# Kernel tuning notes

Measured on AMD Instinct MI355X. Metric: run time of the kernel, lower is better.

## Reference

```python
import jax, jax.numpy as jnp
import numpy as np

B, C, H, W, KS = 8, 3, 512, 512, 3
K = KS * KS  # kernel_elements = 9


def setup_inputs() -> dict:
    key = jax.random.key(0)
    ks = jax.random.split(key, 5)
    return {
        "x": jax.random.normal(ks[0], (B, C, H, W), jnp.float32),
        "w1": jax.random.normal(ks[1], (K - 1, C, KS, KS), jnp.float32) * 0.1,  # find_ref conv weight
        "b1": jax.random.normal(ks[2], (K - 1,), jnp.float32) * 0.1,
        "w2": jax.random.normal(ks[3], (C, K), jnp.float32) * 0.1,  # grouped 1x1 conv: C groups, K in-ch each
        "b2": jax.random.normal(ks[4], (C,), jnp.float32) * 0.1,
    }


def _grid_sample_bilinear(img_nhwc, gx, gy):
    # torch.grid_sample, mode='bilinear', padding_mode='zeros', align_corners=False
    # img_nhwc: [B,H,W,C]; gx,gy: [B,h,w,K] normalized coords (x=width, y=height)
    Bs, Hh, Ww, _ = img_nhwc.shape
    ix = ((gx + 1.0) * Ww - 1.0) * 0.5
    iy = ((gy + 1.0) * Hh - 1.0) * 0.5
    ix0 = jnp.floor(ix)
    iy0 = jnp.floor(iy)
    wx1 = ix - ix0
    wy1 = iy - iy0
    wx0 = 1.0 - wx1
    wy0 = 1.0 - wy1
    bidx = jnp.arange(Bs)[:, None, None, None]

    def corner(yc, xc, wgt):
        valid = (xc >= 0) & (xc < Ww) & (yc >= 0) & (yc < Hh)
        xi = jnp.clip(xc, 0, Ww - 1).astype(jnp.int32)
        yi = jnp.clip(yc, 0, Hh - 1).astype(jnp.int32)
        v = img_nhwc[bidx, yi, xi]  # [B,h,w,K,C]
        return v * (wgt * valid)[..., None]

    out = corner(iy0, ix0, wy0 * wx0)
    out = out + corner(iy0, ix0 + 1.0, wy0 * wx1)
    out = out + corner(iy0 + 1.0, ix0, wy1 * wx0)
    out = out + corner(iy0 + 1.0, ix0 + 1.0, wy1 * wx1)
    return out  # [B,h,w,K,C]


def _forward(x, w1, b1, w2, b2):
    Bs, Cc, Hh, Ww = x.shape
    pad = KS // 2
    # find_ref: conv3x3 (pad=1) + sigmoid -> offsets in [0,1]
    off = jax.lax.conv_general_dilated(
        x, w1, (1, 1), ((pad, pad), (pad, pad)),
        dimension_numbers=("NCHW", "OIHW", "NCHW"))
    off = jax.nn.sigmoid(off + b1[None, :, None, None])  # [B,K-1,H,W]
    off = jnp.transpose(off, (0, 2, 3, 1)).reshape(Bs, Hh, Ww, (K - 1) // 2, 2)
    ctr = float(KS // 2)
    sym = 2.0 * ctr - off  # find_symmetric_points
    center = jnp.zeros((Bs, Hh, Ww, 1, 2), off.dtype)
    off_all = jnp.concatenate([off, center, sym], axis=-2)  # [B,H,W,K,2]
    # base grid: stack(h_grid, w_grid) with linspace(0,1)
    base = jnp.stack(
        jnp.meshgrid(jnp.linspace(0.0, 1.0, Hh), jnp.linspace(0.0, 1.0, Ww), indexing="ij"),
        axis=-1)  # [H,W,2]
    coords = base[None, :, :, None, :] + off_all  # [B,H,W,K,2]
    # grid_sample interprets last dim as (x=width, y=height)
    gx = coords[..., 0]
    gy = coords[..., 1]
    img = jnp.transpose(x, (0, 2, 3, 1))  # [B,H,W,C]
    sampled = _grid_sample_bilinear(img, gx, gy)  # [B,H,W,K,C]
    # concatenation order in torch: elem-major channels -> [B, K*C, H, W]
    deformed = jnp.transpose(sampled, (0, 3, 4, 1, 2)).reshape(Bs, K * Cc, Hh, Ww)
    # grouped 1x1 conv: groups=C, group g consumes channels [g*K:(g+1)*K]
    grp = deformed.reshape(Bs, Cc, K, Hh, Ww)
    out = jnp.einsum("bgkhw,gk->bghw", grp, w2) + b2[None, :, None, None]
    return jax.nn.relu(out)


def reference(x, w1, b1, w2, b2):
    return _forward(x, w1, b1, w2, b2)
```

## Files before the change

### kernel.cpp

```cpp
#include <hip/hip_runtime.h>

#define BATCH 8
#define HDIM  512
#define WDIM  512
#define PLANE (HDIM * WDIM)

typedef _Float16 half4v __attribute__((ext_vector_type(4)));
typedef _Float16 half8v __attribute__((ext_vector_type(8)));

struct __align__(8) HPair { half4v lo, hi; };

__global__ __launch_bounds__(256) void repack_h4(
    const float* __restrict__ x,
    half8v* __restrict__ xp)
{
    int gid = blockIdx.x * 256 + threadIdx.x;
    int b = gid >> 17;
    int u = gid & ((PLANE / 2) - 1);
    const float* xb = x + (size_t)b * 3 * PLANE;
    int pix = u * 2;
    float2 a0 = *(const float2*)(xb + pix);
    float2 a1 = *(const float2*)(xb + PLANE + pix);
    float2 a2 = *(const float2*)(xb + 2 * PLANE + pix);
    half8v o;
    o[0] = (_Float16)a0.x; o[1] = (_Float16)a1.x; o[2] = (_Float16)a2.x; o[3] = (_Float16)0.f;
    o[4] = (_Float16)a0.y; o[5] = (_Float16)a1.y; o[6] = (_Float16)a2.y; o[7] = (_Float16)0.f;
    xp[(size_t)gid] = o;
}

__device__ __forceinline__ void gather5(
    const half4v* __restrict__ hb, const float* __restrict__ w2,
    const float s[8], float bx, float by, float og[3])
{
    int   adr[5][2];
    float wY[5][2], wX0[5], wX1[5];
#pragma unroll
    for (int q = 0; q < 5; q++) {
        float c0 = (q < 4) ? s[2 * q]     : 0.0f;
        float c1 = (q < 4) ? s[2 * q + 1] : 0.0f;
        float ixf = fmaf(bx + c0, 256.0f, 255.5f);
        float iyf = fmaf(by + c1, 256.0f, 255.5f);
        float ix0f = floorf(ixf);
        float iy0f = floorf(iyf);
        float wx1 = ixf - ix0f, wy1 = iyf - iy0f;
        float wx0 = 1.f - wx1,  wy0 = 1.f - wy1;
        int ix0 = (int)ix0f, iy0 = (int)iy0f;

        float wx0v = (ix0 <= 511) ? wx0 : 0.f;
        float wx1v = (ix0 <= 510) ? wx1 : 0.f;
        float wy0v = (iy0 <= 511) ? wy0 : 0.f;
        float wy1v = (iy0 <= 510) ? wy1 : 0.f;
        int x0c = min(ix0, 511);
        int y0c = min(iy0, 511), y1c = min(iy0 + 1, 511);

        float wxs = wx0v + wx1v;
        wX0[q] = wx0v; wX1[q] = wx1v;
        wY[q][0] = wy0v; wY[q][1] = wy1v;
        adr[q][0] = (wy0v * wxs > 0.f) ? ((y0c << 9) + x0c) : 0;
        adr[q][1] = (wy1v * wxs > 0.f) ? ((y1c << 9) + x0c) : 0;
    }

    HPair pv[5][2];
#pragma unroll
    for (int q = 0; q < 5; q++) {
        pv[q][0] = *(const HPair*)(hb + adr[q][0]);
        pv[q][1] = *(const HPair*)(hb + adr[q][1]);
    }

#pragma unroll
    for (int q = 0; q < 5; q++) {
        float sc[3];
#pragma unroll
        for (int c = 0; c < 3; c++) {
            float r0 = fmaf((float)pv[q][0].hi[c], wX1[q], (float)pv[q][0].lo[c] * wX0[q]);
            float r1 = fmaf((float)pv[q][1].hi[c], wX1[q], (float)pv[q][1].lo[c] * wX0[q]);
            sc[c] = fmaf(r1, wY[q][1], r0 * wY[q][0]);
        }
        int g  = q / 3;
        int k0 = (q % 3) * 3;
        og[g] = fmaf(sc[0], w2[g * 9 + k0 + 0], og[g]);
        og[g] = fmaf(sc[1], w2[g * 9 + k0 + 1], og[g]);
        og[g] = fmaf(sc[2], w2[g * 9 + k0 + 2], og[g]);
    }
}

__global__ __launch_bounds__(256) void seesaw_v4(
    const float* __restrict__ x,
    const half4v* __restrict__ xp,
    const float* __restrict__ w1, const float* __restrict__ b1,
    const float* __restrict__ w2, const float* __restrict__ b2,
    float* __restrict__ out)
{
    int t = threadIdx.x;
    int gid = blockIdx.x * 256 + t;
    int u  = gid & 255;
    int j0 = u << 1;
    int i  = (gid >> 8) & 511;
    int b  = gid >> 17;

    const float*  xb = x  + (size_t)b * 3 * PLANE;
    const half4v* hb = xp + ((size_t)b << 18);

    float accA[8], accB[8];
#pragma unroll
    for (int e = 0; e < 8; e++) { accA[e] = b1[e]; accB[e] = b1[e]; }

#pragma unroll
    for (int di = 0; di < 3; di++) {
        int y = i + di - 1;
        bool yv = (unsigned)y < (unsigned)HDIM;
        int yc = yv ? y : 0;
#pragma unroll
        for (int dx = 0; dx < 4; dx++) {
            int xc = j0 + dx - 1;
            bool xv = (unsigned)xc < (unsigned)WDIM;
            int xcc = xv ? xc : 0;
            int base = (yc << 9) + xcc;
            float v0 = xb[base];
            float v1 = xb[PLANE + base];
            float v2 = xb[2 * PLANE + base];
            if (!(yv && xv)) { v0 = 0.f; v1 = 0.f; v2 = 0.f; }
#pragma unroll
            for (int e = 0; e < 8; e++) {
                if (dx < 3) {
                    accA[e] = fmaf(v0, w1[e * 27 +      di * 3 + dx], accA[e]);
                    accA[e] = fmaf(v1, w1[e * 27 +  9 + di * 3 + dx], accA[e]);
                    accA[e] = fmaf(v2, w1[e * 27 + 18 + di * 3 + dx], accA[e]);
                }
                if (dx >= 1) {
                    accB[e] = fmaf(v0, w1[e * 27 +      di * 3 + dx - 1], accB[e]);
                    accB[e] = fmaf(v1, w1[e * 27 +  9 + di * 3 + dx - 1], accB[e]);
                    accB[e] = fmaf(v2, w1[e * 27 + 18 + di * 3 + dx - 1], accB[e]);
                }
            }
        }
    }

    float sA[8], sB[8];
#pragma unroll
    for (int e = 0; e < 8; e++) {
        sA[e] = __builtin_amdgcn_rcpf(1.0f + __expf(-accA[e]));
        sB[e] = __builtin_amdgcn_rcpf(1.0f + __expf(-accB[e]));
    }

    const float inv511 = 1.0f / 511.0f;
    float bx  = (float)i * inv511;
    float byA = (float)j0 * inv511;
    float byB = (float)(j0 + 1) * inv511;

    float ogA[3] = {0.f, 0.f, 0.f};
    float ogB[3] = {0.f, 0.f, 0.f};
    gather5(hb, w2, sA, bx, byA, ogA);
    gather5(hb, w2, sB, bx, byB, ogB);

    if ((i | u) == 0) {
#pragma unroll
        for (int p = 5; p < 9; p++) {
            float c0 = 2.0f - sA[2 * (p - 5)];
            float c1 = 2.0f - sA[2 * (p - 5) + 1];
            float ixf = fmaf(bx + c0, 256.0f, 255.5f);
            float iyf = fmaf(byA + c1, 256.0f, 255.5f);
            float ix0f = floorf(ixf), iy0f = floorf(iyf);
            float wx1 = ixf - ix0f, wy1 = iyf - iy0f;
            float wx0 = 1.f - wx1,  wy0 = 1.f - wy1;
            int ix0 = (int)ix0f, iy0 = (int)iy0f;
            float s0 = 0.f, s1 = 0.f, s2 = 0.f;
            for (int cy = 0; cy < 2; cy++) {
                int yc2 = iy0 + cy;
                if (yc2 < 0 || yc2 >= HDIM) continue;
                float wy = cy ? wy1 : wy0;
                for (int cx = 0; cx < 2; cx++) {
                    int xcc2 = ix0 + cx;
                    if (xcc2 < 0 || xcc2 >= WDIM) continue;
                    float wgt = wy * (cx ? wx1 : wx0);
                    int base = (yc2 << 9) + xcc2;
                    s0 = fmaf(xb[base],             wgt, s0);
                    s1 = fmaf(xb[PLANE + base],     wgt, s1);
                    s2 = fmaf(xb[2 * PLANE + base], wgt, s2);
                }
            }
            int g  = p / 3;
            int k0 = (p % 3) * 3;
            ogA[g] = fmaf(s0, w2[g * 9 + k0 + 0], ogA[g]);
            ogA[g] = fmaf(s1, w2[g * 9 + k0 + 1], ogA[g]);
            ogA[g] = fmaf(s2, w2[g * 9 + k0 + 2], ogA[g]);
        }
    }

    size_t ob = (size_t)(b * 3) * PLANE + ((size_t)i << 9) + j0;
#pragma unroll
    for (int g = 0; g < 3; g++) {
        float va = ogA[g] + b2[g];
        float vb = ogB[g] + b2[g];
        float2 o2;
        o2.x = va > 0.f ? va : 0.f;
        o2.y = vb > 0.f ? vb : 0.f;
        *(float2*)(out + ob + (size_t)g * PLANE) = o2;
    }
}

__global__ __launch_bounds__(256) void seesaw_fused_v1(
    const float* __restrict__ x, const float* __restrict__ w1,
    const float* __restrict__ b1, const float* __restrict__ w2,
    const float* __restrict__ b2, float* __restrict__ out)
{
    int t = threadIdx.x;
    int gid = blockIdx.x * 256 + t;
    int j = gid & (WDIM - 1);
    int i = (gid >> 9) & (HDIM - 1);
    int b = gid >> 18;
    const float* xb = x + (size_t)b * 3 * PLANE;
    float acc[8];
#pragma unroll
    for (int e = 0; e < 8; e++) acc[e] = b1[e];
#pragma unroll
    for (int di = 0; di < 3; di++) {
        int y = i + di - 1;
        if (y < 0 || y >= HDIM) continue;
#pragma unroll
        for (int dj = 0; dj < 3; dj++) {
            int xc = j + dj - 1;
            if (xc < 0 || xc >= WDIM) continue;
            size_t base = (size_t)y * WDIM + xc;
#pragma unroll
            for (int c = 0; c < 3; c++) {
                float v = xb[(size_t)c * PLANE + base];
#pragma unroll
                for (int e = 0; e < 8; e++)
                    acc[e] = fmaf(v, w1[e * 27 + c * 9 + di * 3 + dj], acc[e]);
            }
        }
    }
    float s[8];
#pragma unroll
    for (int e = 0; e < 8; e++) s[e] = 1.0f / (1.0f + __expf(-acc[e]));
    const float inv511 = 1.0f / 511.0f;
    float bx = (float)i * inv511, by = (float)j * inv511;
    float og0 = 0.f, og1 = 0.f, og2 = 0.f;
#pragma unroll
    for (int p = 0; p < 9; p++) {
        float c0, c1;
        if (p < 4)       { c0 = s[2 * p];              c1 = s[2 * p + 1]; }
        else if (p == 4) { c0 = 0.f;                   c1 = 0.f; }
        else             { c0 = 2.0f - s[2 * (p - 5)]; c1 = 2.0f - s[2 * (p - 5) + 1]; }
        float ixf = (bx + c0) * 256.0f + 255.5f;
        float iyf = (by + c1) * 256.0f + 255.5f;
        float ix0f = floorf(ixf), iy0f = floorf(iyf);
        float wx1 = ixf - ix0f, wy1 = iyf - iy0f;
        float wx0 = 1.f - wx1,  wy0 = 1.f - wy1;
        int ix0 = (int)ix0f, iy0 = (int)iy0f;
        float s0 = 0.f, s1 = 0.f, s2 = 0.f;
#pragma unroll
        for (int cy = 0; cy < 2; cy++) {
            int yc = iy0 + cy;
            if (yc < 0 || yc >= HDIM) continue;
            float wy = cy ? wy1 : wy0;
#pragma unroll
            for (int cx = 0; cx < 2; cx++) {
                int xcc = ix0 + cx;
                if (xcc < 0 || xcc >= WDIM) continue;
                float wgt = wy * (cx ? wx1 : wx0);
                size_t base = (size_t)yc * WDIM + xcc;
                s0 = fmaf(xb[base],             wgt, s0);
                s1 = fmaf(xb[PLANE + base],     wgt, s1);
                s2 = fmaf(xb[2 * PLANE + base], wgt, s2);
            }
        }
        int g  = p / 3;
        int k0 = (p % 3) * 3;
        float* og = (g == 0) ? &og0 : (g == 1) ? &og1 : &og2;
        *og = fmaf(s0, w2[g * 9 + k0 + 0], *og);
        *og = fmaf(s1, w2[g * 9 + k0 + 1], *og);
        *og = fmaf(s2, w2[g * 9 + k0 + 2], *og);
    }
    size_t ob = (size_t)(b * 3) * PLANE + (size_t)i * WDIM + j;
    float v0 = og0 + b2[0], v1 = og1 + b2[1], v2 = og2 + b2[2];
    out[ob]             = v0 > 0.f ? v0 : 0.f;
    out[ob + PLANE]     = v1 > 0.f ? v1 : 0.f;
    out[ob + 2 * PLANE] = v2 > 0.f ? v2 : 0.f;
}

extern "C" void kernel_launch(void* const* d_in, const int* in_sizes, int n_in,
                              void* d_out, int out_size, void* d_ws, size_t ws_size,
                              hipStream_t stream) {
    const float* x  = (const float*)d_in[0];
    const float* w1 = (const float*)d_in[1];
    const float* b1 = (const float*)d_in[2];
    const float* w2 = (const float*)d_in[3];
    const float* b2 = (const float*)d_in[4];
    float* out = (float*)d_out;

    int total = BATCH * HDIM * WDIM;
    size_t need = (size_t)total * 8 + 16;

    if (ws_size >= need) {
        half8v* xp = (half8v*)d_ws;
        repack_h4<<<total / 2 / 256, 256, 0, stream>>>(x, xp);
        seesaw_v4<<<total / 2 / 256, 256, 0, stream>>>(x, (const half4v*)d_ws,
                                                       w1, b1, w2, b2, out);
    } else {
        seesaw_fused_v1<<<total / 256, 256, 0, stream>>>(x, w1, b1, w2, b2, out);
    }
}
```

Baseline: 139.1 us.

## Fold grouped 1x1 weights into fp16 dot2 gathers and widen repack

The 1x1 grouped-conv weights are now applied to the packed fp16 channel pairs with fdot2 before bilinear interpolation. This replaces per-channel interpolation followed by a weighted sum, cutting ALU work per sample. The two gather5 calls are merged into one 10-point loop, so all 20 gather loads are issued before any math, giving more loads in flight at the cost of more registers. The repack kernel now handles 4 pixels per thread with float4 loads. The main risk is extra rounding error from fp16 weights.

```diff
diff --git a/kernel.cpp b/kernel.cpp
--- a/kernel.cpp
+++ b/kernel.cpp
@@ -5,88 +5,43 @@
 #define WDIM  512
 #define PLANE (HDIM * WDIM)
 
+typedef _Float16 half2v __attribute__((ext_vector_type(2)));
 typedef _Float16 half4v __attribute__((ext_vector_type(4)));
 typedef _Float16 half8v __attribute__((ext_vector_type(8)));
 
-struct __align__(8) HPair { half4v lo, hi; };
-
-__global__ __launch_bounds__(256) void repack_h4(
+struct __align__(8) HQuad { half2v p0, p1, p2, p3; };
+
+#if __has_builtin(__builtin_amdgcn_fdot2)
+#define FDOT2(a, b, c) __builtin_amdgcn_fdot2((a), (b), (c), false)
+#else
+#define FDOT2(a, b, c) fmaf((float)(a).x, (float)(b).x, fmaf((float)(a).y, (float)(b).y, (c)))
+#endif
+
+__global__ __launch_bounds__(256) void repack_h4w(
     const float* __restrict__ x,
     half8v* __restrict__ xp)
 {
     int gid = blockIdx.x * 256 + threadIdx.x;
-    int b = gid >> 17;
-    int u = gid & ((PLANE / 2) - 1);
+    int b = gid >> 16;
+    int u = gid & 65535;
     const float* xb = x + (size_t)b * 3 * PLANE;
-    int pix = u * 2;
-    float2 a0 = *(const float2*)(xb + pix);
-    float2 a1 = *(const float2*)(xb + PLANE + pix);
-    float2 a2 = *(const float2*)(xb + 2 * PLANE + pix);
-    half8v o;
-    o[0] = (_Float16)a0.x; o[1] = (_Float16)a1.x; o[2] = (_Float16)a2.x; o[3] = (_Float16)0.f;
-    o[4] = (_Float16)a0.y; o[5] = (_Float16)a1.y; o[6] = (_Float16)a2.y; o[7] = (_Float16)0.f;
-    xp[(size_t)gid] = o;
+    int pix = u << 2;
+    float4 a0 = *(const float4*)(xb + pix);
+    float4 a1 = *(const float4*)(xb + PLANE + pix);
+    float4 a2 = *(const float4*)(xb + 2 * PLANE + pix);
+    half8v o0, o1;
+    o0[0] = (_Float16)a0.x; o0[1] = (_Float16)a1.x; o0[2] = (_Float16)a2.x; o0[3] = (_Float16)0.f;
+    o0[4] = (_Float16)a0.y; o0[5] = (_Float16)a1.y; o0[6] = (_Float16)a2.y; o0[7] = (_Float16)0.f;
+    o1[0] = (_Float16)a0.z; o1[1] = (_Float16)a1.z; o1[2] = (_Float16)a2.z; o1[3] = (_Float16)0.f;
+    o1[4] = (_Float16)a0.w; o1[5] = (_Float16)a1.w; o1[6] = (_Float16)a2.w; o1[7] = (_Float16)0.f;
+    size_t base = (size_t)b * (PLANE / 2) + (size_t)u * 2;
+    xp[base]     = o0;
+    xp[base + 1] = o1;
 }
 
-__device__ __forceinline__ void gather5(
-    const half4v* __restrict__ hb, const float* __restrict__ w2,
-    const float s[8], float bx, float by, float og[3])
-{
-    int   adr[5][2];
-    float wY[5][2], wX0[5], wX1[5];
-#pragma unroll
-    for (int q = 0; q < 5; q++) {
-        float c0 = (q < 4) ? s[2 * q]     : 0.0f;
-        float c1 = (q < 4) ? s[2 * q + 1] : 0.0f;
-        float ixf = fmaf(bx + c0, 256.0f, 255.5f);
-        float iyf = fmaf(by + c1, 256.0f, 255.5f);
-        float ix0f = floorf(ixf);
-        float iy0f = floorf(iyf);
-        float wx1 = ixf - ix0f, wy1 = iyf - iy0f;
-        float wx0 = 1.f - wx1,  wy0 = 1.f - wy1;
-        int ix0 = (int)ix0f, iy0 = (int)iy0f;
-
-        float wx0v = (ix0 <= 511) ? wx0 : 0.f;
-        float wx1v = (ix0 <= 510) ? wx1 : 0.f;
-        float wy0v = (iy0 <= 511) ? wy0 : 0.f;
-        float wy1v = (iy0 <= 510) ? wy1 : 0.f;
-        int x0c = min(ix0, 511);
-        int y0c = min(iy0, 511), y1c = min(iy0 + 1, 511);
-
-        float wxs = wx0v + wx1v;
-        wX0[q] = wx0v; wX1[q] = wx1v;
-        wY[q][0] = wy0v; wY[q][1] = wy1v;
-        adr[q][0] = (wy0v * wxs > 0.f) ? ((y0c << 9) + x0c) : 0;
-        adr[q][1] = (wy1v * wxs > 0.f) ? ((y1c << 9) + x0c) : 0;
-    }
-
-    HPair pv[5][2];
-#pragma unroll
-    for (int q = 0; q < 5; q++) {
-        pv[q][0] = *(const HPair*)(hb + adr[q][0]);
-        pv[q][1] = *(const HPair*)(hb + adr[q][1]);
-    }
-
-#pragma unroll
-    for (int q = 0; q < 5; q++) {
-        float sc[3];
-#pragma unroll
-        for (int c = 0; c < 3; c++) {
-            float r0 = fmaf((float)pv[q][0].hi[c], wX1[q], (float)pv[q][0].lo[c] * wX0[q]);
-            float r1 = fmaf((float)pv[q][1].hi[c], wX1[q], (float)pv[q][1].lo[c] * wX0[q]);
-            sc[c] = fmaf(r1, wY[q][1], r0 * wY[q][0]);
-        }
-        int g  = q / 3;
-        int k0 = (q % 3) * 3;
-        og[g] = fmaf(sc[0], w2[g * 9 + k0 + 0], og[g]);
-        og[g] = fmaf(sc[1], w2[g * 9 + k0 + 1], og[g]);
-        og[g] = fmaf(sc[2], w2[g * 9 + k0 + 2], og[g]);
-    }
-}
-
-__global__ __launch_bounds__(256) void seesaw_v4(
+__global__ __launch_bounds__(256) void seesaw_v5(
     const float* __restrict__ x,
-    const half4v* __restrict__ xp,
+    const char* __restrict__ xpack,
     const float* __restrict__ w1, const float* __restrict__ b1,
     const float* __restrict__ w2, const float* __restrict__ b2,
     float* __restrict__ out)
@@ -98,8 +53,8 @@
     int i  = (gid >> 8) & 511;
     int b  = gid >> 17;
 
-    const float*  xb = x  + (size_t)b * 3 * PLANE;
-    const half4v* hb = xp + ((size_t)b << 18);
+    const float* xb = x + (size_t)b * 3 * PLANE;
+    const char*  hb = xpack + ((size_t)b << 21);
 
     float accA[8], accB[8];
 #pragma unroll
@@ -143,15 +98,72 @@
         sB[e] = __builtin_amdgcn_rcpf(1.0f + __expf(-accB[e]));
     }
 
+    half2v w2a[5], w2b[5];
+#pragma unroll
+    for (int q = 0; q < 5; q++) {
+        w2a[q][0] = (_Float16)w2[q * 3];
+        w2a[q][1] = (_Float16)w2[q * 3 + 1];
+        w2b[q][0] = (_Float16)w2[q * 3 + 2];
+        w2b[q][1] = (_Float16)0.f;
+    }
+
     const float inv511 = 1.0f / 511.0f;
     float bx  = (float)i * inv511;
     float byA = (float)j0 * inv511;
     float byB = (float)(j0 + 1) * inv511;
 
-    float ogA[3] = {0.f, 0.f, 0.f};
-    float ogB[3] = {0.f, 0.f, 0.f};
-    gather5(hb, w2, sA, bx, byA, ogA);
-    gather5(hb, w2, sB, bx, byB, ogB);
+    int   adr[10][2];
+    float wY0[10], wY1[10], wX0[10], wX1[10];
+#pragma unroll
+    for (int q = 0; q < 10; q++) {
+        int pp = q % 5;
+        const float* sv = (q < 5) ? sA : sB;
+        float by = (q < 5) ? byA : byB;
+        float c0 = (pp < 4) ? sv[2 * pp]     : 0.0f;
+        float c1 = (pp < 4) ? sv[2 * pp + 1] : 0.0f;
+        float ixf = fmaf(bx + c0, 256.0f, 255.5f);
+        float iyf = fmaf(by + c1, 256.0f, 255.5f);
+        float ix0f = floorf(ixf);
+        float iy0f = floorf(iyf);
+        float wx1 = ixf - ix0f, wy1 = iyf - iy0f;
+        float wx0 = 1.f - wx1,  wy0 = 1.f - wy1;
+        int ix0 = (int)ix0f, iy0 = (int)iy0f;
+
+        float wx0v = (ix0 <= 511) ? wx0 : 0.f;
+        float wx1v = (ix0 <= 510) ? wx1 : 0.f;
+        float wy0v = (iy0 <= 511) ? wy0 : 0.f;
+        float wy1v = (iy0 <= 510) ? wy1 : 0.f;
+        int x0c = min(ix0, 511);
+        int y0c = min(iy0, 511), y1c = min(iy0 + 1, 511);
+
+        float wxs = wx0v + wx1v;
+        wX0[q] = wx0v; wX1[q] = wx1v;
+        wY0[q] = wy0v; wY1[q] = wy1v;
+        adr[q][0] = (wy0v * wxs > 0.f) ? ((y0c << 9) + x0c) : 0;
+        adr[q][1] = (wy1v * wxs > 0.f) ? ((y1c << 9) + x0c) : 0;
+    }
+
+    HQuad qv[10][2];
+#pragma unroll
+    for (int q = 0; q < 10; q++) {
+        qv[q][0] = *(const HQuad*)(hb + ((size_t)adr[q][0] << 3));
+        qv[q][1] = *(const HQuad*)(hb + ((size_t)adr[q][1] << 3));
+    }
+
+    float og[2][3] = {{0.f, 0.f, 0.f}, {0.f, 0.f, 0.f}};
+#pragma unroll
+    for (int q = 0; q < 10; q++) {
+        int pp = q % 5;
+        int px = q / 5;
+        int g  = pp / 3;
+        float dl0 = FDOT2(qv[q][0].p0, w2a[pp], FDOT2(qv[q][0].p1, w2b[pp], 0.f));
+        float dh0 = FDOT2(qv[q][0].p2, w2a[pp], FDOT2(qv[q][0].p3, w2b[pp], 0.f));
+        float dl1 = FDOT2(qv[q][1].p0, w2a[pp], FDOT2(qv[q][1].p1, w2b[pp], 0.f));
+        float dh1 = FDOT2(qv[q][1].p2, w2a[pp], FDOT2(qv[q][1].p3, w2b[pp], 0.f));
+        float r0 = fmaf(dh0, wX1[q], dl0 * wX0[q]);
+        float r1 = fmaf(dh1, wX1[q], dl1 * wX0[q]);
+        og[px][g] = fmaf(r1, wY1[q], fmaf(r0, wY0[q], og[px][g]));
+    }
 
     if ((i | u) == 0) {
 #pragma unroll
@@ -181,17 +193,17 @@
             }
             int g  = p / 3;
             int k0 = (p % 3) * 3;
-            ogA[g] = fmaf(s0, w2[g * 9 + k0 + 0], ogA[g]);
-            ogA[g] = fmaf(s1, w2[g * 9 + k0 + 1], ogA[g]);
-            ogA[g] = fmaf(s2, w2[g * 9 + k0 + 2], ogA[g]);
+            og[0][g] = fmaf(s0, w2[g * 9 + k0 + 0], og[0][g]);
+            og[0][g] = fmaf(s1, w2[g * 9 + k0 + 1], og[0][g]);
+            og[0][g] = fmaf(s2, w2[g * 9 + k0 + 2], og[0][g]);
         }
     }
 
     size_t ob = (size_t)(b * 3) * PLANE + ((size_t)i << 9) + j0;
 #pragma unroll
     for (int g = 0; g < 3; g++) {
-        float va = ogA[g] + b2[g];
-        float vb = ogB[g] + b2[g];
+        float va = og[0][g] + b2[g];
+        float vb = og[1][g] + b2[g];
         float2 o2;
         o2.x = va > 0.f ? va : 0.f;
         o2.y = vb > 0.f ? vb : 0.f;
@@ -294,9 +306,8 @@
     size_t need = (size_t)total * 8 + 16;
 
     if (ws_size >= need) {
-        half8v* xp = (half8v*)d_ws;
-        repack_h4<<<total / 2 / 256, 256, 0, stream>>>(x, xp);
-        seesaw_v4<<<total / 2 / 256, 256, 0, stream>>>(x, (const half4v*)d_ws,
+        repack_h4w<<<total / 4 / 256, 256, 0, stream>>>(x, (half8v*)d_ws);
+        seesaw_v5<<<total / 2 / 256, 256, 0, stream>>>(x, (const char*)d_ws,
                                                        w1, b1, w2, b2, out);
     } else {
         seesaw_fused_v1<<<total / 256, 256, 0, stream>>>(x, w1, b1, w2, b2, out);
```

Result: no change. 137.8 us (-1.0%).
